# Optimization experiments

Measured on AMD Instinct MI355X. Metric: run time of the kernel, lower is better.

Reference implementation:

```python
import jax, jax.numpy as jnp
import numpy as np

WEIGHT_BIT = 8
BIAS_BIT = 32
EPS = 1e-8


def setup_inputs() -> dict:
    key = jax.random.key(0)
    k1, k2, k3, k4 = jax.random.split(key, 4)
    N, IN, OUT = 65536, 512, 512
    # x_q: already-quantized int8-range activations stored as float32
    x_q = jax.random.randint(k1, (N, IN), -128, 128).astype(jnp.float32)
    weight = jax.random.normal(k2, (OUT, IN), dtype=jnp.float32) * 0.05
    bias = jax.random.normal(k3, (OUT,), dtype=jnp.float32) * 0.01
    scale_x = jax.random.uniform(k4, (1,), dtype=jnp.float32, minval=0.01, maxval=0.1)
    return {"x_q": x_q, "weight": weight, "bias": bias, "scale_x": scale_x}


def _symmetric_quant_weight(w, bit):
    # per-output-channel symmetric quantization (min/max over dim=1)
    n = float(2 ** (bit - 1) - 1)  # 127 for 8-bit
    sat = jnp.maximum(jnp.abs(w.min(axis=1)), jnp.abs(w.max(axis=1)))  # [OUT]
    scale = jnp.maximum(sat, EPS) / n                                   # [OUT]
    w_q = jnp.clip(jnp.round(w / scale[:, None]), -n - 1.0, n)
    return w_q, scale


def reference(x_q, weight, bias, scale_x):
    w_q, scale_w = _symmetric_quant_weight(weight, WEIGHT_BIT)
    scale_out = scale_w * scale_x[0]          # [OUT] per-channel output scale
    nb = float(2 ** (BIAS_BIT - 1) - 1)
    b_q = jnp.clip(jnp.round(bias / scale_out), -nb - 1.0, nb)
    # integer-only matmul: int32 GEMM with int32 bias
    out_q = (jnp.dot(x_q.astype(jnp.int32), w_q.astype(jnp.int32).T)
             + b_q.astype(jnp.int32)[None, :])
    return out_q, scale_out.reshape(1, -1)
```

## Files before the change

kernel.cpp:

```cpp
#include <hip/hip_runtime.h>
#include <hip/hip_bf16.h>

typedef __attribute__((ext_vector_type(8))) short bf16x8;
typedef __attribute__((ext_vector_type(4))) float f32x4;

#define KDIM 512
#define NDIM 512
#define BM 128
#define BN 128
#define WROWS 32
#define BK 64
#define NT (KDIM / BK)

__device__ __forceinline__ unsigned int pack_bf16(float a, float b) {
  return (__builtin_bit_cast(unsigned int, a) >> 16) |
         (__builtin_bit_cast(unsigned int, b) & 0xffff0000u);
}

__global__ __launch_bounds__(64)
void quant_w_kernel(const float* __restrict__ W, const float* __restrict__ bias,
                    const float* __restrict__ scale_x,
                    ushort* __restrict__ Wq_arr, float* __restrict__ bq,
                    float* __restrict__ so_out) {
  const int n = blockIdx.x;
  const int l = threadIdx.x;
  const float* row = W + (size_t)n * KDIM;
  float4 v0 = *(const float4*)(row + l * 8);
  float4 v1 = *(const float4*)(row + l * 8 + 4);
  float m = fmaxf(fmaxf(fmaxf(fabsf(v0.x), fabsf(v0.y)), fmaxf(fabsf(v0.z), fabsf(v0.w))),
                  fmaxf(fmaxf(fabsf(v1.x), fabsf(v1.y)), fmaxf(fabsf(v1.z), fabsf(v1.w))));
#pragma unroll
  for (int off = 32; off; off >>= 1) m = fmaxf(m, __shfl_xor(m, off, 64));
  const float scale = fmaxf(m, 1e-8f) / 127.0f;
  float vals[8] = {v0.x, v0.y, v0.z, v0.w, v1.x, v1.y, v1.z, v1.w};
  unsigned int packed[4];
#pragma unroll
  for (int i = 0; i < 4; ++i) {
    float qa = fminf(fmaxf(rintf(vals[2 * i] / scale), -128.f), 127.f);
    float qb = fminf(fmaxf(rintf(vals[2 * i + 1] / scale), -128.f), 127.f);
    packed[i] = pack_bf16(qa, qb);
  }
  const size_t slot = ((size_t)(n >> 4) * 16 + (l >> 2)) * 64 + (n & 15) + (l & 3) * 16;
  *(uint4*)(Wq_arr + slot * 8) = make_uint4(packed[0], packed[1], packed[2], packed[3]);
  if (l == 0) {
    float so = scale * scale_x[0];
    so_out[n] = so;
    bq[n] = rintf(bias[n] / so);
  }
}

__global__ __launch_bounds__(256, 3)
void gemm_kernel(const float* __restrict__ X, const ushort* __restrict__ Wqa,
                 const float* __restrict__ bq, float* __restrict__ Out) {
  __shared__ __align__(16) char smem[4][8192];

  const int nblk = gridDim.x;
  int swz = blockIdx.x;
  if ((nblk & 7) == 0)
    swz = (blockIdx.x & 7) * (nblk >> 3) + (blockIdx.x >> 3);
  const int bm = swz >> 2;
  const int bn = swz & 3;

  const int tid = threadIdx.x;
  const int l = tid & 63, w = tid >> 6;
  const int lr = l & 15, lk = l >> 4;

  const int wrow0 = bm * BM + w * WROWS;
  const float* xbase = X + (size_t)wrow0 * KDIM;
  char* sA = smem[w];

  f32x4 acc[2][8];
#pragma unroll
  for (int i = 0; i < 2; ++i)
#pragma unroll
    for (int j = 0; j < 8; ++j) acc[i][j] = (f32x4){0.f, 0.f, 0.f, 0.f};

  float4 raw[8];
  auto gloadA = [&](int t) {
#pragma unroll
    for (int i = 0; i < 8; ++i)
      raw[i] = *(const float4*)(xbase + (size_t)(i * 4 + lk) * KDIM + t * BK + lr * 4);
  };
  auto packwrite = [&](char* buf) {
#pragma unroll
    for (int i = 0; i < 8; ++i) {
      int lrow = i * 4 + lk;
      int byteo = (lrow * 128 + lr * 8) ^ ((lrow & 7) << 4);
      uint2 p;
      p.x = pack_bf16(raw[i].x, raw[i].y);
      p.y = pack_bf16(raw[i].z, raw[i].w);
      *(uint2*)(buf + byteo) = p;
    }
  };
  auto readA = [&](const char* buf, int mf, int ks) -> bf16x8 {
    int lrow = mf * 16 + lr;
    int byteo = (lrow * 128 + (ks * 4 + lk) * 16) ^ ((lrow & 7) << 4);
    return *(const bf16x8*)(buf + byteo);
  };

  gloadA(0);
  packwrite(sA);
  gloadA(1);

  for (int t = 0; t < NT; ++t) {
    char* bufc = sA + (t & 1) * 4096;
    char* bufn = sA + ((t + 1) & 1) * 4096;
    bf16x8 af[2][2];
#pragma unroll
    for (int mf = 0; mf < 2; ++mf)
#pragma unroll
      for (int ks = 0; ks < 2; ++ks) af[mf][ks] = readA(bufc, mf, ks);
    if (t < NT - 1) packwrite(bufn);
#pragma unroll
    for (int ks = 0; ks < 2; ++ks) {
      const int kt = t * 2 + ks;
      bf16x8 bf[8];
#pragma unroll
      for (int nf = 0; nf < 8; ++nf)
        bf[nf] = *(const bf16x8*)(Wqa + (((size_t)(bn * 8 + nf) * 16 + kt) * 64 + l) * 8);
#pragma unroll
      for (int mf = 0; mf < 2; ++mf)
#pragma unroll
        for (int nf = 0; nf < 8; ++nf)
          acc[mf][nf] = __builtin_amdgcn_mfma_f32_16x16x32_bf16(af[mf][ks], bf[nf],
                                                                acc[mf][nf], 0, 0, 0);
    }
    if (t < NT - 2) gloadA(t + 2);
  }

  float bqv[8];
#pragma unroll
  for (int nf = 0; nf < 8; ++nf) bqv[nf] = bq[bn * BN + nf * 16 + lr];

  float* fs = (float*)sA;
#pragma unroll
  for (int mf = 0; mf < 2; ++mf) {
#pragma unroll
    for (int nf = 0; nf < 8; ++nf) {
      const int col = nf * 16 + lr;
#pragma unroll
      for (int e = 0; e < 4; ++e) {
        int r = lk * 4 + e;
        fs[r * 128 + (col ^ ((r & 12) << 2))] = acc[mf][nf][e] + bqv[nf];
      }
    }
#pragma unroll
    for (int j = 0; j < 8; ++j) {
      const int r = j * 2 + (l >> 5);
      const int c4 = (l & 31) * 4;
      f32x4 v = *(const f32x4*)(fs + r * 128 + (c4 ^ ((r & 12) << 2)));
      *(f32x4*)(Out + (size_t)(wrow0 + mf * 16 + r) * NDIM + bn * BN + c4) = v;
    }
  }
}

extern "C" void kernel_launch(void* const* d_in, const int* in_sizes, int n_in,
                              void* d_out, int out_size, void* d_ws, size_t ws_size,
                              hipStream_t stream) {
  const float* x = (const float*)d_in[0];
  const float* weight = (const float*)d_in[1];
  const float* bias = (const float*)d_in[2];
  const float* scale_x = (const float*)d_in[3];
  const int M = in_sizes[0] / KDIM;

  float* out = (float*)d_out;
  float* so_out = out + (size_t)M * NDIM;
  ushort* Wq_arr = (ushort*)d_ws;
  float* bq = (float*)((char*)d_ws + (size_t)NDIM * KDIM * sizeof(ushort));

  quant_w_kernel<<<NDIM, 64, 0, stream>>>(weight, bias, scale_x, Wq_arr, bq, so_out);

  const int blocks = (M / BM) * (NDIM / BN);
  gemm_kernel<<<blocks, 256, 0, stream>>>(x, Wq_arr, bq, out);
}
```

Before: 346.7 us.

## Drop LDS staging, load A directly into MFMA fragments with narrower N tiles

Removes the shared-memory staging of the activation tile, so each lane loads its A fragment straight from global memory and packs it to bf16 in registers. The block's N tile is halved to 64 columns (twice as many blocks), B fragments are double-buffered in registers, and the epilogue writes scalar outputs directly instead of transposing through LDS. The aim is to cut LDS traffic and register pressure so four blocks fit per CU. In exchange, each activation row is now read by eight blocks instead of four, the global A loads are less coalesced, and the output stores are scalar and strided.

```diff
diff --git a/kernel.cpp b/kernel.cpp
--- a/kernel.cpp
+++ b/kernel.cpp
@@ -6,11 +6,7 @@
 
 #define KDIM 512
 #define NDIM 512
-#define BM 128
-#define BN 128
-#define WROWS 32
-#define BK 64
-#define NT (KDIM / BK)
+#define NKT 16
 
 __device__ __forceinline__ unsigned int pack_bf16(float a, float b) {
   return (__builtin_bit_cast(unsigned int, a) >> 16) |
@@ -49,109 +45,86 @@
   }
 }
 
-__global__ __launch_bounds__(256, 3)
+__global__ __launch_bounds__(256, 4)
 void gemm_kernel(const float* __restrict__ X, const ushort* __restrict__ Wqa,
                  const float* __restrict__ bq, float* __restrict__ Out) {
-  __shared__ __align__(16) char smem[4][8192];
-
   const int nblk = gridDim.x;
   int swz = blockIdx.x;
   if ((nblk & 7) == 0)
     swz = (blockIdx.x & 7) * (nblk >> 3) + (blockIdx.x >> 3);
-  const int bm = swz >> 2;
-  const int bn = swz & 3;
+  const int bm = swz >> 3;
+  const int bn = swz & 7;
 
   const int tid = threadIdx.x;
   const int l = tid & 63, w = tid >> 6;
   const int lr = l & 15, lk = l >> 4;
 
-  const int wrow0 = bm * BM + w * WROWS;
-  const float* xbase = X + (size_t)wrow0 * KDIM;
-  char* sA = smem[w];
+  const int wrow0 = bm * 128 + w * 32;
+  const int nc0 = bn * 4;
 
-  f32x4 acc[2][8];
+  const float* x0 = X + (size_t)(wrow0 + lr) * KDIM + lk * 8;
+  const float* x1 = x0 + (size_t)16 * KDIM;
+  const ushort* bbase = Wqa + ((size_t)nc0 * 16 * 64 + l) * 8;
+
+  f32x4 acc[2][4];
 #pragma unroll
   for (int i = 0; i < 2; ++i)
 #pragma unroll
-    for (int j = 0; j < 8; ++j) acc[i][j] = (f32x4){0.f, 0.f, 0.f, 0.f};
+    for (int j = 0; j < 4; ++j) acc[i][j] = (f32x4){0.f, 0.f, 0.f, 0.f};
 
-  float4 raw[8];
-  auto gloadA = [&](int t) {
+  float4 Ab[2][4];
+  bf16x8 Bb[2][4];
+
+  auto loadA = [&](int kt, int buf) {
+    Ab[buf][0] = *(const float4*)(x0 + kt * 32);
+    Ab[buf][1] = *(const float4*)(x0 + kt * 32 + 4);
+    Ab[buf][2] = *(const float4*)(x1 + kt * 32);
+    Ab[buf][3] = *(const float4*)(x1 + kt * 32 + 4);
+  };
+  auto loadB = [&](int kt, int buf) {
 #pragma unroll
-    for (int i = 0; i < 8; ++i)
-      raw[i] = *(const float4*)(xbase + (size_t)(i * 4 + lk) * KDIM + t * BK + lr * 4);
-  };
-  auto packwrite = [&](char* buf) {
-#pragma unroll
-    for (int i = 0; i < 8; ++i) {
-      int lrow = i * 4 + lk;
-      int byteo = (lrow * 128 + lr * 8) ^ ((lrow & 7) << 4);
-      uint2 p;
-      p.x = pack_bf16(raw[i].x, raw[i].y);
-      p.y = pack_bf16(raw[i].z, raw[i].w);
-      *(uint2*)(buf + byteo) = p;
-    }
-  };
-  auto readA = [&](const char* buf, int mf, int ks) -> bf16x8 {
-    int lrow = mf * 16 + lr;
-    int byteo = (lrow * 128 + (ks * 4 + lk) * 16) ^ ((lrow & 7) << 4);
-    return *(const bf16x8*)(buf + byteo);
+    for (int nf = 0; nf < 4; ++nf)
+      Bb[buf][nf] = *(const bf16x8*)(bbase + ((size_t)nf * 16 + kt) * 512);
   };
 
-  gloadA(0);
-  packwrite(sA);
-  gloadA(1);
+  loadA(0, 0); loadB(0, 0);
+  loadA(1, 1); loadB(1, 1);
 
-  for (int t = 0; t < NT; ++t) {
-    char* bufc = sA + (t & 1) * 4096;
-    char* bufn = sA + ((t + 1) & 1) * 4096;
-    bf16x8 af[2][2];
 #pragma unroll
-    for (int mf = 0; mf < 2; ++mf)
+  for (int kt = 0; kt < NKT; ++kt) {
+    const int cur = kt & 1;
+    bf16x8 af[2];
 #pragma unroll
-      for (int ks = 0; ks < 2; ++ks) af[mf][ks] = readA(bufc, mf, ks);
-    if (t < NT - 1) packwrite(bufn);
+    for (int mf = 0; mf < 2; ++mf) {
+      float4 a0 = Ab[cur][mf * 2], a1 = Ab[cur][mf * 2 + 1];
+      union { unsigned int u[4]; bf16x8 v; } r;
+      r.u[0] = pack_bf16(a0.x, a0.y);
+      r.u[1] = pack_bf16(a0.z, a0.w);
+      r.u[2] = pack_bf16(a1.x, a1.y);
+      r.u[3] = pack_bf16(a1.z, a1.w);
+      af[mf] = r.v;
+    }
+    if (kt + 2 < NKT) loadA(kt + 2, cur);
 #pragma unroll
-    for (int ks = 0; ks < 2; ++ks) {
-      const int kt = t * 2 + ks;
-      bf16x8 bf[8];
-#pragma unroll
-      for (int nf = 0; nf < 8; ++nf)
-        bf[nf] = *(const bf16x8*)(Wqa + (((size_t)(bn * 8 + nf) * 16 + kt) * 64 + l) * 8);
-#pragma unroll
-      for (int mf = 0; mf < 2; ++mf)
-#pragma unroll
-        for (int nf = 0; nf < 8; ++nf)
-          acc[mf][nf] = __builtin_amdgcn_mfma_f32_16x16x32_bf16(af[mf][ks], bf[nf],
-                                                                acc[mf][nf], 0, 0, 0);
+    for (int nf = 0; nf < 4; ++nf) {
+      acc[0][nf] = __builtin_amdgcn_mfma_f32_16x16x32_bf16(af[0], Bb[cur][nf], acc[0][nf], 0, 0, 0);
+      acc[1][nf] = __builtin_amdgcn_mfma_f32_16x16x32_bf16(af[1], Bb[cur][nf], acc[1][nf], 0, 0, 0);
     }
-    if (t < NT - 2) gloadA(t + 2);
+    if (kt + 2 < NKT) loadB(kt + 2, cur);
   }
 
-  float bqv[8];
+  const int colb = bn * 64;
+  float bqv[4];
 #pragma unroll
-  for (int nf = 0; nf < 8; ++nf) bqv[nf] = bq[bn * BN + nf * 16 + lr];
-
-  float* fs = (float*)sA;
+  for (int nf = 0; nf < 4; ++nf) bqv[nf] = bq[colb + nf * 16 + lr];
+  float* outp = Out + (size_t)(wrow0 + lk * 4) * NDIM + colb + lr;
 #pragma unroll
-  for (int mf = 0; mf < 2; ++mf) {
+  for (int mf = 0; mf < 2; ++mf)
 #pragma unroll
-    for (int nf = 0; nf < 8; ++nf) {
-      const int col = nf * 16 + lr;
+    for (int nf = 0; nf < 4; ++nf)
 #pragma unroll
-      for (int e = 0; e < 4; ++e) {
-        int r = lk * 4 + e;
-        fs[r * 128 + (col ^ ((r & 12) << 2))] = acc[mf][nf][e] + bqv[nf];
-      }
-    }
-#pragma unroll
-    for (int j = 0; j < 8; ++j) {
-      const int r = j * 2 + (l >> 5);
-      const int c4 = (l & 31) * 4;
-      f32x4 v = *(const f32x4*)(fs + r * 128 + (c4 ^ ((r & 12) << 2)));
-      *(f32x4*)(Out + (size_t)(wrow0 + mf * 16 + r) * NDIM + bn * BN + c4) = v;
-    }
-  }
+      for (int e = 0; e < 4; ++e)
+        outp[(size_t)(mf * 16 + e) * NDIM + nf * 16] = acc[mf][nf][e] + bqv[nf];
 }
 
 extern "C" void kernel_launch(void* const* d_in, const int* in_sizes, int n_in,
@@ -170,6 +143,6 @@
 
   quant_w_kernel<<<NDIM, 64, 0, stream>>>(weight, bias, scale_x, Wq_arr, bq, so_out);
 
-  const int blocks = (M / BM) * (NDIM / BN);
+  const int blocks = (M / 128) * (NDIM / 64);
   gemm_kernel<<<blocks, 256, 0, stream>>>(x, Wq_arr, bq, out);
 }
```

Result: slower. 368.9 us (+6.4%).
